# Performance work log

Hardware: AMD Instinct MI355X
Metric: run time of the kernel (lower is better)

## Reference

```python
import jax, jax.numpy as jnp
import numpy as np


def setup_inputs() -> dict:
    key = jax.random.key(0)
    k1, k2 = jax.random.split(key)
    B, S, HOP, L = 32, 524288, 256, 100
    frames = S // HOP
    # input hook asserts 0 <= phase <= 0.5
    wrapped_phase = jax.random.uniform(k1, (B, S), dtype=jnp.float32) * 0.5
    tables = jax.random.normal(k2, (B, frames + 1, L), dtype=jnp.float32)
    return {"wrapped_phase": wrapped_phase, "tables": tables, "hop_length": HOP}


def reference(wrapped_phase, tables, hop_length):
    # wrapped_phase: (B, S), hop_length divides S; tables: (B, S//hop + 1, L)
    B, S = wrapped_phase.shape
    frames = S // hop_length
    L = tables.shape[2]

    wp = wrapped_phase.reshape(B, frames, hop_length)          # (B, F, H)
    idx_raw = wp * L
    floor_idx = jnp.clip(idx_raw.astype(jnp.int32), 0, L - 1)  # (B, F, H)
    p = idx_raw - floor_idx.astype(wp.dtype)                   # frac along table axis

    # wrap-around pad of one sample along table axis: (B, F+1, L+1)
    padded = jnp.concatenate([tables, tables[:, :, :1]], axis=2)
    floor_flow = padded[:, :-1]                                # (B, F, L+1) frame t
    ceil_flow = padded[:, 1:]                                  # (B, F, L+1) frame t+1

    def lerp_table(flow):
        lo = jnp.take_along_axis(flow, floor_idx, axis=2)
        hi = jnp.take_along_axis(flow, floor_idx + 1, axis=2)
        return lo * (1 - p) + hi * p

    sel_floor = lerp_table(floor_flow)                         # (B, F, H)
    sel_ceil = lerp_table(ceil_flow)

    # interpolate across hop (frame) dimension
    p2 = jnp.arange(hop_length, dtype=wp.dtype) / hop_length   # (H,)
    final = sel_floor * (1 - p2) + sel_ceil * p2
    return final.reshape(B, -1)[:, :S]
```

## Files before the change

kernel.cpp:

```cpp
#include <hip/hip_runtime.h>

constexpr int HOP    = 256;
constexpr int L      = 100;
constexpr int FRAMES = 2048;
constexpr int B      = 32;
constexpr int FPB    = 4;

__global__ __launch_bounds__(256) void glottal_kernel(
    const float* __restrict__ wp,
    const float* __restrict__ tables,
    float* __restrict__ out)
{
    __shared__ float2 pairs[FPB][L + 1];

    const int tid = threadIdx.x;
    const int b   = blockIdx.x >> 9;
    const int g   = blockIdx.x & 511;
    const int f0  = g * FPB;

    const float* trow = tables + ((size_t)b * (FRAMES + 1) + (size_t)f0) * L;

    for (int i = tid; i < FPB * (L + 1); i += 256) {
        int r  = i / (L + 1);
        int c  = i - r * (L + 1);
        int cs = (c == L) ? 0 : c;
        pairs[r][c] = make_float2(trow[r * L + cs], trow[(r + 1) * L + cs]);
    }
    __syncthreads();

    const size_t base = ((size_t)b * FRAMES + (size_t)f0) * HOP + (size_t)tid * 4;
    float4 w = *reinterpret_cast<const float4*>(wp + base);

    const float2* row = pairs[tid >> 6];
    const int h0 = (tid & 63) * 4;

    float wv[4] = {w.x, w.y, w.z, w.w};
    float res[4];
#pragma unroll
    for (int j = 0; j < 4; ++j) {
        float idx_raw = wv[j] * (float)L;
        int fi = (int)idx_raw;
        fi = fi < 0 ? 0 : (fi > L - 1 ? L - 1 : fi);
        float p  = idx_raw - (float)fi;
        float2 lo = row[fi];
        float2 hi = row[fi + 1];
        float sf = lo.x + (hi.x - lo.x) * p;
        float sc = lo.y + (hi.y - lo.y) * p;
        float p2 = (float)(h0 + j) * (1.0f / HOP);
        res[j] = sf + (sc - sf) * p2;
    }

    *reinterpret_cast<float4*>(out + base) = make_float4(res[0], res[1], res[2], res[3]);
}

extern "C" void kernel_launch(void* const* d_in, const int* in_sizes, int n_in,
                              void* d_out, int out_size, void* d_ws, size_t ws_size,
                              hipStream_t stream) {
    const float* wp     = (const float*)d_in[0];
    const float* tables = (const float*)d_in[1];
    float* out = (float*)d_out;

    dim3 grid(B * (FRAMES / FPB));
    glottal_kernel<<<grid, 256, 0, stream>>>(wp, tables, out);
}
```

Before: 135.3 us.

## Process sixteen frames per block with hoisted phase loads and deduplicated table reads

Each block now handles 16 frames instead of 4, which cuts the grid to a quarter of its size. All four float4 phase loads are issued up front, before the table staging, so their latency overlaps with the shared-memory fill. The table fill reads each table row once and writes it into both the .x slot of frame r and the .y slot of frame r-1, which removes the duplicated global reads. The trade-offs are fewer blocks to spread across CUs and more registers per thread.

```diff
diff --git a/kernel.cpp b/kernel.cpp
--- a/kernel.cpp
+++ b/kernel.cpp
@@ -4,7 +4,8 @@
 constexpr int L      = 100;
 constexpr int FRAMES = 2048;
 constexpr int B      = 32;
-constexpr int FPB    = 4;
+constexpr int FPB    = 16;
+constexpr int GPB    = FRAMES / FPB;
 
 __global__ __launch_bounds__(256) void glottal_kernel(
     const float* __restrict__ wp,
@@ -14,43 +15,51 @@
     __shared__ float2 pairs[FPB][L + 1];
 
     const int tid = threadIdx.x;
-    const int b   = blockIdx.x >> 9;
-    const int g   = blockIdx.x & 511;
+    const int b   = blockIdx.x >> 7;
+    const int g   = blockIdx.x & (GPB - 1);
     const int f0  = g * FPB;
 
+    const size_t blockbase = ((size_t)b * FRAMES + (size_t)f0) * HOP;
+
+    float4 w[4];
+#pragma unroll
+    for (int j = 0; j < 4; ++j)
+        w[j] = *reinterpret_cast<const float4*>(wp + blockbase + j * 1024 + tid * 4);
+
     const float* trow = tables + ((size_t)b * (FRAMES + 1) + (size_t)f0) * L;
-
-    for (int i = tid; i < FPB * (L + 1); i += 256) {
+    for (int i = tid; i < (FPB + 1) * (L + 1); i += 256) {
         int r  = i / (L + 1);
         int c  = i - r * (L + 1);
         int cs = (c == L) ? 0 : c;
-        pairs[r][c] = make_float2(trow[r * L + cs], trow[(r + 1) * L + cs]);
+        float v = trow[r * L + cs];
+        if (r < FPB) pairs[r][c].x = v;
+        if (r > 0)   pairs[r - 1][c].y = v;
     }
     __syncthreads();
 
-    const size_t base = ((size_t)b * FRAMES + (size_t)f0) * HOP + (size_t)tid * 4;
-    float4 w = *reinterpret_cast<const float4*>(wp + base);
-
-    const float2* row = pairs[tid >> 6];
     const int h0 = (tid & 63) * 4;
-
-    float wv[4] = {w.x, w.y, w.z, w.w};
-    float res[4];
 #pragma unroll
     for (int j = 0; j < 4; ++j) {
-        float idx_raw = wv[j] * (float)L;
-        int fi = (int)idx_raw;
-        fi = fi < 0 ? 0 : (fi > L - 1 ? L - 1 : fi);
-        float p  = idx_raw - (float)fi;
-        float2 lo = row[fi];
-        float2 hi = row[fi + 1];
-        float sf = lo.x + (hi.x - lo.x) * p;
-        float sc = lo.y + (hi.y - lo.y) * p;
-        float p2 = (float)(h0 + j) * (1.0f / HOP);
-        res[j] = sf + (sc - sf) * p2;
+        const float2* row = pairs[j * 4 + (tid >> 6)];
+
+        float wv[4] = {w[j].x, w[j].y, w[j].z, w[j].w};
+        float res[4];
+#pragma unroll
+        for (int k = 0; k < 4; ++k) {
+            float idx_raw = wv[k] * (float)L;
+            int fi = (int)idx_raw;
+            fi = fi < 0 ? 0 : (fi > L - 1 ? L - 1 : fi);
+            float p  = idx_raw - (float)fi;
+            float2 lo = row[fi];
+            float2 hi = row[fi + 1];
+            float sf = lo.x + (hi.x - lo.x) * p;
+            float sc = lo.y + (hi.y - lo.y) * p;
+            float p2 = (float)(h0 + k) * (1.0f / HOP);
+            res[k] = sf + (sc - sf) * p2;
+        }
+        *reinterpret_cast<float4*>(out + blockbase + j * 1024 + tid * 4) =
+            make_float4(res[0], res[1], res[2], res[3]);
     }
-
-    *reinterpret_cast<float4*>(out + base) = make_float4(res[0], res[1], res[2], res[3]);
 }
 
 extern "C" void kernel_launch(void* const* d_in, const int* in_sizes, int n_in,
@@ -60,6 +69,6 @@
     const float* tables = (const float*)d_in[1];
     float* out = (float*)d_out;
 
-    dim3 grid(B * (FRAMES / FPB));
+    dim3 grid(B * GPB);
     glottal_kernel<<<grid, 256, 0, stream>>>(wp, tables, out);
 }
```

After: 140.2 us. 1.04x slower.

## Process eight frame groups per block with double-buffered async table staging

Applied to the files above, without the earlier changes.

Each block now handles eight consecutive frame groups instead of one. The table rows for the next group go into a second LDS buffer with global_load_lds while the current group is computed, and the next phase vector is prefetched into registers. The LDS layout changes from interleaved float2 pairs with an explicit wrap column to a plain copy of five table rows. This drops the per-element index arithmetic during staging and cuts the block count. The wrap column and the lower clamp are removed, which is only correct because phases are bounded by 0.5; a per-iteration barrier is added.

```diff
diff --git a/kernel.cpp b/kernel.cpp
--- a/kernel.cpp
+++ b/kernel.cpp
@@ -5,52 +5,77 @@
 constexpr int FRAMES = 2048;
 constexpr int B      = 32;
 constexpr int FPB    = 4;
+constexpr int GPR    = FRAMES / FPB;
+constexpr int GROUPS = B * GPR;
+constexpr int GPBLK  = 8;
+constexpr int NBLK   = GROUPS / GPBLK;
+
+constexpr int TABF   = (FPB + 1) * L;
+
+typedef const __attribute__((address_space(1))) void gvoid;
+typedef __attribute__((address_space(3)))       void svoid;
 
 __global__ __launch_bounds__(256) void glottal_kernel(
     const float* __restrict__ wp,
     const float* __restrict__ tables,
     float* __restrict__ out)
 {
-    __shared__ float2 pairs[FPB][L + 1];
+    __shared__ float tab[2][TABF];
 
-    const int tid = threadIdx.x;
-    const int b   = blockIdx.x >> 9;
-    const int g   = blockIdx.x & 511;
-    const int f0  = g * FPB;
+    const int tid  = threadIdx.x;
+    const int wv   = tid >> 6;
+    const int lane = tid & 63;
+    const int grp0 = blockIdx.x * GPBLK;
 
-    const float* trow = tables + ((size_t)b * (FRAMES + 1) + (size_t)f0) * L;
+    const float4* wp4  = reinterpret_cast<const float4*>(wp);
+    float4*       out4 = reinterpret_cast<float4*>(out);
 
-    for (int i = tid; i < FPB * (L + 1); i += 256) {
-        int r  = i / (L + 1);
-        int c  = i - r * (L + 1);
-        int cs = (c == L) ? 0 : c;
-        pairs[r][c] = make_float2(trow[r * L + cs], trow[(r + 1) * L + cs]);
-    }
+    auto stage_tab = [&](int g, int pp) {
+        if (tid < TABF / 4) {
+            const int b = g >> 9;
+            const int r = g & (GPR - 1);
+            const float* src = tables
+                + ((size_t)b * (FRAMES + 1) + (size_t)r * FPB) * L + tid * 4;
+            __builtin_amdgcn_global_load_lds((gvoid*)src,
+                                             (svoid*)&tab[pp][tid * 4], 16, 0, 0);
+        }
+    };
+
+    stage_tab(grp0, 0);
+    float4 wnext = wp4[(size_t)grp0 * 256 + tid];
     __syncthreads();
 
-    const size_t base = ((size_t)b * FRAMES + (size_t)f0) * HOP + (size_t)tid * 4;
-    float4 w = *reinterpret_cast<const float4*>(wp + base);
+    for (int it = 0; it < GPBLK; ++it) {
+        const int pp  = it & 1;
+        const int grp = grp0 + it;
+        const float4 w = wnext;
 
-    const float2* row = pairs[tid >> 6];
-    const int h0 = (tid & 63) * 4;
+        if (it + 1 < GPBLK) {
+            wnext = wp4[(size_t)(grp + 1) * 256 + tid];
+            stage_tab(grp + 1, pp ^ 1);
+        }
 
-    float wv[4] = {w.x, w.y, w.z, w.w};
-    float res[4];
+        const float* trow = &tab[pp][wv * L];
+        const float  wv4[4] = {w.x, w.y, w.z, w.w};
+        const float  p2b = (float)(lane * 4) * (1.0f / HOP);
+        float res[4];
 #pragma unroll
-    for (int j = 0; j < 4; ++j) {
-        float idx_raw = wv[j] * (float)L;
-        int fi = (int)idx_raw;
-        fi = fi < 0 ? 0 : (fi > L - 1 ? L - 1 : fi);
-        float p  = idx_raw - (float)fi;
-        float2 lo = row[fi];
-        float2 hi = row[fi + 1];
-        float sf = lo.x + (hi.x - lo.x) * p;
-        float sc = lo.y + (hi.y - lo.y) * p;
-        float p2 = (float)(h0 + j) * (1.0f / HOP);
-        res[j] = sf + (sc - sf) * p2;
+        for (int k = 0; k < 4; ++k) {
+            const float ir = wv4[k] * (float)L;
+            int fi = (int)ir;
+            fi = fi > L - 1 ? L - 1 : fi;
+            const float p   = ir - (float)fi;
+            const float lo0 = trow[fi],     lo1 = trow[fi + 1];
+            const float hi0 = trow[fi + L], hi1 = trow[fi + L + 1];
+            const float sf  = lo0 + (lo1 - lo0) * p;
+            const float sc  = hi0 + (hi1 - hi0) * p;
+            res[k] = sf + (sc - sf) * (p2b + (float)k * (1.0f / HOP));
+        }
+
+        out4[(size_t)grp * 256 + tid] = make_float4(res[0], res[1], res[2], res[3]);
+
+        __syncthreads();
     }
-
-    *reinterpret_cast<float4*>(out + base) = make_float4(res[0], res[1], res[2], res[3]);
 }
 
 extern "C" void kernel_launch(void* const* d_in, const int* in_sizes, int n_in,
@@ -60,6 +85,6 @@
     const float* tables = (const float*)d_in[1];
     float* out = (float*)d_out;
 
-    dim3 grid(B * (FRAMES / FPB));
+    dim3 grid(NBLK);
     glottal_kernel<<<grid, 256, 0, stream>>>(wp, tables, out);
 }
```

After: 137.1 us. Within noise of the previous version (+1.3%).
